# Kernel optimization log

Hardware: AMD Instinct MI355X
Metric: run time of the kernel (lower is better)

## Reference

```python
import jax, jax.numpy as jnp
import numpy as np

# Module hyperparameters (init_kwargs)
KH, KW = 1, 1            # kernel_size
PATCH_H, PATCH_W = 21, 21  # patch_size (displacement grid)
SH, SW = 1, 1            # stride
PAD_H, PAD_W = 0, 0      # padding
DILP_H, DILP_W = 1, 1    # dilation_patch
B, C, H, W = 8, 256, 64, 96


def setup_inputs() -> dict:
    key = jax.random.key(0)
    k1, k2 = jax.random.split(key)
    input1 = jax.random.normal(k1, (B, C, H, W), dtype=jnp.float32)
    input2 = jax.random.normal(k2, (B, C, H, W), dtype=jnp.float32)
    return {"input1": input1, "input2": input2}


def _correlation(x1, x2):
    """FlowNet-style spatial correlation (cost volume).

    out[b, pi, pj, i, j] = sum_{c, ki, kj}
        x1_pad[b, c, i*SH + ki, j*SW + kj] *
        x2_pad[b, c, i*SH + ki + (pi - radH)*DILP_H, j*SW + kj + (pj - radW)*DILP_W]
    Out-of-bounds reads of x2 are zero (handled by padding).
    """
    radH, radW = PATCH_H // 2, PATCH_W // 2
    x1p = jnp.pad(x1, ((0, 0), (0, 0), (PAD_H, PAD_H), (PAD_W, PAD_W)))
    x2p = jnp.pad(x2, ((0, 0), (0, 0),
                       (PAD_H + radH * DILP_H, PAD_H + radH * DILP_H),
                       (PAD_W + radW * DILP_W, PAD_W + radW * DILP_W)))
    Hp, Wp = H + 2 * PAD_H, W + 2 * PAD_W
    oH = (Hp - KH) // SH + 1
    oW = (Wp - KW) // SW + 1

    # displacement grid -> start offsets into x2p (0 corresponds to -rad shift)
    sh = jnp.arange(PATCH_H, dtype=jnp.int32) * DILP_H
    sw = jnp.arange(PATCH_W, dtype=jnp.int32) * DILP_W
    starts = jnp.stack(jnp.meshgrid(sh, sw, indexing="ij"), axis=-1).reshape(-1, 2)

    def step(carry, s):
        # shifted view of x2 aligned with padded x1
        sl = jax.lax.dynamic_slice(x2p, (0, 0, s[0], s[1]), (B, C, Hp, Wp))
        prod = jnp.sum(x1p * sl, axis=1)  # [B, Hp, Wp], channel reduction
        # kernel-window sum + output stride (KH=KW=1 -> single strided slice)
        acc = jnp.zeros((B, oH, oW), dtype=prod.dtype)
        for ki in range(KH):
            for kj in range(KW):
                acc = acc + jax.lax.slice(
                    prod, (0, ki, kj),
                    (B, ki + (oH - 1) * SH + 1, kj + (oW - 1) * SW + 1),
                    (1, SH, SW))
        return carry, acc

    _, out = jax.lax.scan(step, None, starts)  # [PATCH_H*PATCH_W, B, oH, oW]
    out = out.reshape(PATCH_H, PATCH_W, B, oH, oW)
    return jnp.transpose(out, (2, 0, 1, 3, 4))  # [B, patchH, patchW, oH, oW]


def reference(input1, input2):
    return _correlation(input1, input2)
```

## Files before the change

kernel.cpp:

```cpp
#include <hip/hip_runtime.h>

typedef __attribute__((ext_vector_type(8))) short short8;
typedef __attribute__((ext_vector_type(4))) float f32x4;
typedef __attribute__((ext_vector_type(4))) unsigned short us4;

constexpr int NB = 8, NC = 256, IH = 64, IW = 96;
constexpr int PATCH = 21, RAD = 10;
constexpr int TI = 8, TJ = 8;
constexpr int WIN = 28, NWIN = 784;
constexpr int KC = 32, NKS = NC / KC;
constexpr int PLANE = IH * IW;
constexpr int PH = IH + 2 * RAD, PW = IW + 2 * RAD;
constexpr int NBCH = NWIN * 4;
constexpr int NCHUNK = NBCH + 256;
constexpr int ASTR = IH * IW * KC;
constexpr int BSTR = PH * PW * KC;
constexpr size_t X1T_ELEMS = (size_t)NB * NKS * ASTR;
constexpr size_t X2P_ELEMS = (size_t)NB * NKS * BSTR;
constexpr int GSTR = 65;

__device__ __forceinline__ unsigned short f2bf(float f) {
  unsigned u = __builtin_bit_cast(unsigned, f);
  u += 0x7fffu + ((u >> 16) & 1u);
  return (unsigned short)(u >> 16);
}

__global__ __launch_bounds__(256) void x1_to_kmajor(
    const float* __restrict__ src, unsigned short* __restrict__ dst) {
  __shared__ float lsf[32 * 97];
  const int blk = blockIdx.x;
  const int ct = blk & 7, i = (blk >> 3) & 63, b = blk >> 9;
  const int c0 = ct * 32, t = threadIdx.x;
  const float* sp = src + ((size_t)b * NC + c0) * PLANE + (size_t)i * IW;
#pragma unroll
  for (int k = 0; k < 12; ++k) {
    int idx = k * 256 + t;
    int c = idx / 96, j = idx - c * 96;
    lsf[c * 97 + j] = sp[(size_t)c * PLANE + j];
  }
  __syncthreads();
  unsigned short* dp = dst + (((size_t)(b * NKS + ct) * IH + i) * IW) * KC;
#pragma unroll
  for (int k = 0; k < 3; ++k) {
    int o = k * 256 + t;
    int j = o >> 3, cq = o & 7;
    us4 v = {f2bf(lsf[(cq * 4 + 0) * 97 + j]), f2bf(lsf[(cq * 4 + 1) * 97 + j]),
             f2bf(lsf[(cq * 4 + 2) * 97 + j]), f2bf(lsf[(cq * 4 + 3) * 97 + j])};
    *(us4*)&dp[(size_t)j * KC + cq * 4] = v;
  }
}

__global__ __launch_bounds__(256) void x2_to_kmajor_pad(
    const float* __restrict__ src, unsigned short* __restrict__ dst) {
  __shared__ float lsf[32 * 97];
  const int blk = blockIdx.x;
  const int ct = blk & 7, i = (blk >> 3) % PH, b = blk / (PH * 8);
  const int c0 = ct * 32, t = threadIdx.x;
  const int isrc = i - RAD;
  const bool rowok = (unsigned)isrc < (unsigned)IH;
  if (rowok) {
    const float* sp = src + ((size_t)b * NC + c0) * PLANE + (size_t)isrc * IW;
#pragma unroll
    for (int k = 0; k < 12; ++k) {
      int idx = k * 256 + t;
      int c = idx / 96, j = idx - c * 96;
      lsf[c * 97 + j] = sp[(size_t)c * PLANE + j];
    }
  }
  __syncthreads();
  unsigned short* dp = dst + (((size_t)(b * NKS + ct) * PH + i) * PW) * KC;
#pragma unroll
  for (int k = 0; k < 4; ++k) {
    int o = k * 256 + t;
    if (o < PW * 8) {
      int j = o >> 3, cq = o & 7;
      int jsrc = j - RAD;
      us4 v = {0, 0, 0, 0};
      if (rowok && (unsigned)jsrc < (unsigned)IW)
        v = us4{f2bf(lsf[(cq * 4 + 0) * 97 + jsrc]), f2bf(lsf[(cq * 4 + 1) * 97 + jsrc]),
                f2bf(lsf[(cq * 4 + 2) * 97 + jsrc]), f2bf(lsf[(cq * 4 + 3) * 97 + jsrc])};
      *(us4*)&dp[(size_t)j * KC + cq * 4] = v;
    }
  }
}

__global__ __launch_bounds__(1024, 4) void corr_pipe16(
    const unsigned short* __restrict__ x1k, const unsigned short* __restrict__ x2k,
    float* __restrict__ out) {
  __shared__ __attribute__((aligned(16))) unsigned short ls[3 * NCHUNK * 8];

  const int t = threadIdx.x, lane = t & 63, wv = t >> 6;
  const int bid = blockIdx.x;
  const int b = bid & 7;
  const int tile = bid >> 3;
  const int ti = tile / 12, tj = tile - ti * 12;
  const int i0 = ti * TI, j0 = tj * TJ;
  const int mtp = wv & 1, cg = wv >> 1;
  const int cbeg = cg * 6;
  const int qk = lane >> 4, lr = lane & 15;

  const unsigned short* x1b = x1k + (size_t)b * NKS * ASTR;
  const unsigned short* x2b = x2k + (size_t)b * NKS * BSTR;

  const unsigned short* srcp[4];
#pragma unroll
  for (int it = 0; it < 4; ++it) {
    int q = it * 1024 + t;
    if (q < NBCH) {
      int w = ((q >> 3) << 1) | (((q >> 2) ^ (q >> 4)) & 1);
      int c4 = (q & 3) ^ (w & 3);
      int wi = w / WIN, wj = w - wi * WIN;
      srcp[it] = x2b + ((size_t)(i0 + wi) * PW + (j0 + wj)) * KC + c4 * 8;
    } else {
      int qa = (q - NBCH) & 255;
      int m = ((qa >> 3) << 1) | (((qa >> 2) ^ (qa >> 4)) & 1);
      int c4 = (qa & 3) ^ (m & 3);
      srcp[it] = x1b + ((size_t)(i0 + (m >> 3)) * IW + (j0 + (m & 7))) * KC + c4 * 8;
    }
  }

  f32x4 acc[2][7];
#pragma unroll
  for (int a = 0; a < 2; ++a)
#pragma unroll
    for (int cc = 0; cc < 7; ++cc) acc[a][cc] = (f32x4){0.f, 0.f, 0.f, 0.f};

#define STAGE(BUF, KS)                                                              \
  {                                                                                 \
    unsigned short* lb = &ls[(BUF) * NCHUNK * 8];                                   \
    _Pragma("unroll")                                                               \
    for (int it = 0; it < 3; ++it)                                                  \
      __builtin_amdgcn_global_load_lds(                                             \
          (const void*)(srcp[it] + (size_t)(KS) * BSTR),                            \
          (void*)(lb + (it * 1024 + wv * 64) * 8), 16, 0, 0);                       \
    if (wv < 5)                                                                     \
      __builtin_amdgcn_global_load_lds(                                             \
          (const void*)(srcp[3] + (size_t)(KS) * (wv == 0 ? BSTR : ASTR)),          \
          (void*)(lb + (3072 + wv * 64) * 8), 16, 0, 0);                            \
  }

#define COMPUTE(BUF)                                                                \
  {                                                                                 \
    const unsigned short* lb = &ls[(BUF) * NCHUNK * 8];                             \
    const int m0 = 32 * mtp + lr, m1 = m0 + 16;                                     \
    short8 a0 = *(const short8*)(lb + (NBCH + ((4 * m0 + qk) ^ (lr & 7))) * 8);     \
    short8 a1 = *(const short8*)(lb + (NBCH + ((4 * m1 + qk) ^ (lr & 7))) * 8);     \
    _Pragma("unroll")                                                               \
    for (int cc = 0; cc < 7; ++cc) {                                                \
      int wrow = 16 * (cbeg + cc) + lr;                                             \
      int slot = (4 * wrow + qk) ^ (lr & 7);                                        \
      short8 bf = *(const short8*)(lb + slot * 8);                                  \
      acc[0][cc] = __builtin_amdgcn_mfma_f32_16x16x32_bf16(a0, bf, acc[0][cc], 0, 0, 0); \
      acc[1][cc] = __builtin_amdgcn_mfma_f32_16x16x32_bf16(a1, bf, acc[1][cc], 0, 0, 0); \
    }                                                                               \
  }

  STAGE(0, 0)
  STAGE(1, 1)

#define ITER(KS, VMA, VMB)                                        \
  if ((KS) < 6) STAGE((KS + 2) % 3, KS + 2)                       \
  if (wv < 5) { asm volatile("s_waitcnt vmcnt(" #VMA ")" ::: "memory"); }  \
  else        { asm volatile("s_waitcnt vmcnt(" #VMB ")" ::: "memory"); }  \
  asm volatile("s_barrier" ::: "memory");                         \
  COMPUTE(KS % 3)                                                 \
  asm volatile("s_barrier" ::: "memory");

  ITER(0, 8, 6)
  ITER(1, 8, 6)
  ITER(2, 8, 6)
  ITER(3, 8, 6)
  ITER(4, 8, 6)
  ITER(5, 8, 6)
  ITER(6, 4, 3)
  ITER(7, 0, 0)
#undef ITER
#undef COMPUTE
#undef STAGE

  float* gf = (float*)ls;
#pragma unroll
  for (int ch = 0; ch < 2; ++ch) {
    __syncthreads();
    const int n0 = ch ? 384 : 0;
#pragma unroll
    for (int a = 0; a < 2; ++a)
#pragma unroll
      for (int cc = 0; cc < 7; ++cc) {
        int ccg = cbeg + cc;
        if (ch ? (ccg >= 24) : (ccg <= 24)) {
          int nl = 16 * ccg + lr - n0;
          int mb = 16 * (2 * mtp + a) + 4 * qk;
          float* gp = &gf[nl * GSTR + mb];
          gp[0] = acc[a][cc][0]; gp[1] = acc[a][cc][1];
          gp[2] = acc[a][cc][2]; gp[3] = acc[a][cc][3];
        }
      }
    __syncthreads();
    for (int s = t; s < 1764; s += 1024) {
      int pidx = s / 21, pj = s - pidx * 21;
      int ii = 0, rem = pidx, stop = 0;
#pragma unroll
      for (int k = 0; k < 7; ++k) {
        int cnt = ch ? (7 + k) : (14 - k);
        int go = (!stop) && (rem >= cnt);
        rem -= go ? cnt : 0;
        ii += go;
        stop |= !go;
      }
      int pi = ch ? (14 - ii + rem) : rem;
      int nl = 28 * (pi + ii) + pj - n0;
      int ms = 8 * ii;
      float g[8];
#pragma unroll
      for (int e = 0; e < 8; ++e) g[e] = gf[(nl + e) * GSTR + ms + e];
      float* op = out + ((((size_t)b * PATCH + pi) * PATCH + pj) * IH + (i0 + ii)) * IW + j0;
      f32x4 v0 = {g[0], g[1], g[2], g[3]};
      f32x4 v1 = {g[4], g[5], g[6], g[7]};
      *(f32x4*)op = v0;
      *(f32x4*)(op + 4) = v1;
    }
  }
}

constexpr int LDKF = 40;
__global__ __launch_bounds__(512, 2) void corr_mfma_fb(
    const float* __restrict__ x1, const float* __restrict__ x2, float* __restrict__ out) {
  __shared__ __attribute__((aligned(16))) unsigned short lsA[64 * LDKF];
  __shared__ __attribute__((aligned(16))) unsigned short lsB[NWIN * LDKF];
  const int t = threadIdx.x;
  const int b = blockIdx.y;
  const int ti = blockIdx.x / 12, tj = blockIdx.x % 12;
  const int i0 = ti * TI, j0 = tj * TJ;
  const int lane = t & 63, wv = t >> 6;
  const int mtp = wv >> 2, cg = wv & 3, cbeg = cg * 12;
  const int qk = lane >> 4, lr = lane & 15;
  f32x4 acc[2][13];
#pragma unroll
  for (int a = 0; a < 2; ++a)
#pragma unroll
    for (int cc = 0; cc < 13; ++cc) acc[a][cc] = (f32x4){0.f, 0.f, 0.f, 0.f};
  const int am = t & 63, ak4 = t >> 6;
  const int aii = am >> 3, ajj = am & 7;
  const float* x1p = x1 + ((size_t)b * NC + 4 * ak4) * PLANE + (size_t)(i0 + aii) * IW + (j0 + ajj);
  const float* x2b = x2 + (size_t)b * NC * PLANE;
  for (int ks = 0; ks < NKS; ++ks) {
    __syncthreads();
    {
      const float* p = x1p + (size_t)ks * KC * PLANE;
      us4 v = {f2bf(p[0]), f2bf(p[PLANE]), f2bf(p[2 * PLANE]), f2bf(p[3 * PLANE])};
      *(us4*)&lsA[am * LDKF + 4 * ak4] = v;
    }
    for (int w = t; w < NWIN; w += 512) {
      const int wi = w / WIN, wj = w - wi * WIN;
      const int gi = i0 - RAD + wi, gj = j0 - RAD + wj;
      const bool ok = ((unsigned)gi < (unsigned)IH) && ((unsigned)gj < (unsigned)IW);
      const float* p = x2b + ((size_t)(ks * KC) * IH + gi) * IW + gj;
      unsigned short* dst = &lsB[w * LDKF];
#pragma unroll
      for (int k4 = 0; k4 < 8; ++k4) {
        const float* q = p + (size_t)(4 * k4) * PLANE;
        us4 v = {f2bf(ok ? q[0] : 0.f), f2bf(ok ? q[PLANE] : 0.f),
                 f2bf(ok ? q[2 * PLANE] : 0.f), f2bf(ok ? q[3 * PLANE] : 0.f)};
        *(us4*)&dst[4 * k4] = v;
      }
    }
    __syncthreads();
    short8 a0 = *(const short8*)&lsA[(32 * mtp + lr) * LDKF + 8 * qk];
    short8 a1 = *(const short8*)&lsA[(32 * mtp + 16 + lr) * LDKF + 8 * qk];
#pragma unroll
    for (int cc = 0; cc < 13; ++cc) {
      const int wrow = 16 * (cbeg + cc) + lr;
      short8 bf = *(const short8*)&lsB[wrow * LDKF + 8 * qk];
      acc[0][cc] = __builtin_amdgcn_mfma_f32_16x16x32_bf16(a0, bf, acc[0][cc], 0, 0, 0);
      acc[1][cc] = __builtin_amdgcn_mfma_f32_16x16x32_bf16(a1, bf, acc[1][cc], 0, 0, 0);
    }
  }
#pragma unroll
  for (int a = 0; a < 2; ++a) {
    const int mb = 16 * (2 * mtp + a) + qk * 4;
#pragma unroll
    for (int cc = 0; cc < 13; ++cc) {
      if (cg > 0 && cc == 0) continue;
      const int n = 16 * (cbeg + cc) + lr;
      const int wi = n / WIN, wj = n - wi * WIN;
#pragma unroll
      for (int r = 0; r < 4; ++r) {
        const int m = mb + r;
        const int ii = m >> 3, jj = m & 7;
        const int pi = wi - ii, pj = wj - jj;
        if ((unsigned)pi < (unsigned)PATCH && (unsigned)pj < (unsigned)PATCH)
          out[((((size_t)b * PATCH + pi) * PATCH + pj) * IH + (i0 + ii)) * IW + (j0 + jj)] =
              acc[a][cc][r];
      }
    }
  }
}

extern "C" void kernel_launch(void* const* d_in, const int* in_sizes, int n_in,
                              void* d_out, int out_size, void* d_ws, size_t ws_size,
                              hipStream_t stream) {
  const float* x1 = (const float*)d_in[0];
  const float* x2 = (const float*)d_in[1];
  float* out = (float*)d_out;
  const size_t need = (X1T_ELEMS + X2P_ELEMS) * sizeof(unsigned short);
  if (ws_size >= need) {
    unsigned short* x1k = (unsigned short*)d_ws;
    unsigned short* x2k = x1k + X1T_ELEMS;
    x1_to_kmajor<<<NB * IH * 8, 256, 0, stream>>>(x1, x1k);
    x2_to_kmajor_pad<<<NB * PH * 8, 256, 0, stream>>>(x2, x2k);
    corr_pipe16<<<NB * 96, 1024, 0, stream>>>(x1k, x2k, out);
  } else {
    dim3 grid(96, NB);
    corr_mfma_fb<<<grid, 512, 0, stream>>>(x1, x2, out);
  }
}
```

Before: 95.13 us.

## Halve block to 8 waves, each wave covering all four M tiles

The correlation kernel now runs with 512 threads (8 waves) instead of 1024. Each wave keeps all four 16-row A fragments and 4x7 accumulators, so the B fragments loaded from LDS are reused across four MFMAs instead of two. Staging loads are redistributed with 7 source pointers per thread and a uniform vmcnt wait. This cuts LDS read traffic per MFMA but doubles accumulator registers and halves the number of waves available to hide latency.

New measurement: 86.13 us. -9.5%, faster.

```diff
diff --git a/kernel.cpp b/kernel.cpp
--- a/kernel.cpp
+++ b/kernel.cpp
@@ -84,7 +84,7 @@
   }
 }
 
-__global__ __launch_bounds__(1024, 4) void corr_pipe16(
+__global__ __launch_bounds__(512, 2) void corr_pipe8(
     const unsigned short* __restrict__ x1k, const unsigned short* __restrict__ x2k,
     float* __restrict__ out) {
   __shared__ __attribute__((aligned(16))) unsigned short ls[3 * NCHUNK * 8];
@@ -95,17 +95,16 @@
   const int tile = bid >> 3;
   const int ti = tile / 12, tj = tile - ti * 12;
   const int i0 = ti * TI, j0 = tj * TJ;
-  const int mtp = wv & 1, cg = wv >> 1;
-  const int cbeg = cg * 6;
+  const int cbeg = 6 * wv;
   const int qk = lane >> 4, lr = lane & 15;
 
   const unsigned short* x1b = x1k + (size_t)b * NKS * ASTR;
   const unsigned short* x2b = x2k + (size_t)b * NKS * BSTR;
 
-  const unsigned short* srcp[4];
-#pragma unroll
-  for (int it = 0; it < 4; ++it) {
-    int q = it * 1024 + t;
+  const unsigned short* srcp[7];
+#pragma unroll
+  for (int it = 0; it < 7; ++it) {
+    int q = it * 512 + t;
     if (q < NBCH) {
       int w = ((q >> 3) << 1) | (((q >> 2) ^ (q >> 4)) & 1);
       int c4 = (q & 3) ^ (w & 3);
@@ -119,9 +118,9 @@
     }
   }
 
-  f32x4 acc[2][7];
-#pragma unroll
-  for (int a = 0; a < 2; ++a)
+  f32x4 acc[4][7];
+#pragma unroll
+  for (int a = 0; a < 4; ++a)
 #pragma unroll
     for (int cc = 0; cc < 7; ++cc) acc[a][cc] = (f32x4){0.f, 0.f, 0.f, 0.f};
 
@@ -129,51 +128,53 @@
   {                                                                                 \
     unsigned short* lb = &ls[(BUF) * NCHUNK * 8];                                   \
     _Pragma("unroll")                                                               \
-    for (int it = 0; it < 3; ++it)                                                  \
+    for (int it = 0; it < 6; ++it)                                                  \
       __builtin_amdgcn_global_load_lds(                                             \
           (const void*)(srcp[it] + (size_t)(KS) * BSTR),                            \
-          (void*)(lb + (it * 1024 + wv * 64) * 8), 16, 0, 0);                       \
+          (void*)(lb + (it * 512 + wv * 64) * 8), 16, 0, 0);                        \
     if (wv < 5)                                                                     \
       __builtin_amdgcn_global_load_lds(                                             \
-          (const void*)(srcp[3] + (size_t)(KS) * (wv == 0 ? BSTR : ASTR)),          \
+          (const void*)(srcp[6] + (size_t)(KS) * (wv == 0 ? BSTR : ASTR)),          \
           (void*)(lb + (3072 + wv * 64) * 8), 16, 0, 0);                            \
   }
 
 #define COMPUTE(BUF)                                                                \
   {                                                                                 \
     const unsigned short* lb = &ls[(BUF) * NCHUNK * 8];                             \
-    const int m0 = 32 * mtp + lr, m1 = m0 + 16;                                     \
-    short8 a0 = *(const short8*)(lb + (NBCH + ((4 * m0 + qk) ^ (lr & 7))) * 8);     \
-    short8 a1 = *(const short8*)(lb + (NBCH + ((4 * m1 + qk) ^ (lr & 7))) * 8);     \
+    short8 af0 = *(const short8*)(lb + (NBCH + ((4 * (lr) + qk) ^ (lr & 7))) * 8);        \
+    short8 af1 = *(const short8*)(lb + (NBCH + ((4 * (16 + lr) + qk) ^ (lr & 7))) * 8);   \
+    short8 af2 = *(const short8*)(lb + (NBCH + ((4 * (32 + lr) + qk) ^ (lr & 7))) * 8);   \
+    short8 af3 = *(const short8*)(lb + (NBCH + ((4 * (48 + lr) + qk) ^ (lr & 7))) * 8);   \
     _Pragma("unroll")                                                               \
     for (int cc = 0; cc < 7; ++cc) {                                                \
       int wrow = 16 * (cbeg + cc) + lr;                                             \
       int slot = (4 * wrow + qk) ^ (lr & 7);                                        \
       short8 bf = *(const short8*)(lb + slot * 8);                                  \
-      acc[0][cc] = __builtin_amdgcn_mfma_f32_16x16x32_bf16(a0, bf, acc[0][cc], 0, 0, 0); \
-      acc[1][cc] = __builtin_amdgcn_mfma_f32_16x16x32_bf16(a1, bf, acc[1][cc], 0, 0, 0); \
+      acc[0][cc] = __builtin_amdgcn_mfma_f32_16x16x32_bf16(af0, bf, acc[0][cc], 0, 0, 0); \
+      acc[1][cc] = __builtin_amdgcn_mfma_f32_16x16x32_bf16(af1, bf, acc[1][cc], 0, 0, 0); \
+      acc[2][cc] = __builtin_amdgcn_mfma_f32_16x16x32_bf16(af2, bf, acc[2][cc], 0, 0, 0); \
+      acc[3][cc] = __builtin_amdgcn_mfma_f32_16x16x32_bf16(af3, bf, acc[3][cc], 0, 0, 0); \
     }                                                                               \
   }
 
   STAGE(0, 0)
   STAGE(1, 1)
 
-#define ITER(KS, VMA, VMB)                                        \
-  if ((KS) < 6) STAGE((KS + 2) % 3, KS + 2)                       \
-  if (wv < 5) { asm volatile("s_waitcnt vmcnt(" #VMA ")" ::: "memory"); }  \
-  else        { asm volatile("s_waitcnt vmcnt(" #VMB ")" ::: "memory"); }  \
-  asm volatile("s_barrier" ::: "memory");                         \
-  COMPUTE(KS % 3)                                                 \
+#define ITER(KS, VM)                                           \
+  if ((KS) < 6) STAGE((KS + 2) % 3, KS + 2)                    \
+  asm volatile("s_waitcnt vmcnt(" #VM ")" ::: "memory");       \
+  asm volatile("s_barrier" ::: "memory");                      \
+  COMPUTE(KS % 3)                                              \
   asm volatile("s_barrier" ::: "memory");
 
-  ITER(0, 8, 6)
-  ITER(1, 8, 6)
-  ITER(2, 8, 6)
-  ITER(3, 8, 6)
-  ITER(4, 8, 6)
-  ITER(5, 8, 6)
-  ITER(6, 4, 3)
-  ITER(7, 0, 0)
+  ITER(0, 12)
+  ITER(1, 12)
+  ITER(2, 12)
+  ITER(3, 12)
+  ITER(4, 12)
+  ITER(5, 12)
+  ITER(6, 6)
+  ITER(7, 0)
 #undef ITER
 #undef COMPUTE
 #undef STAGE
@@ -184,20 +185,20 @@
     __syncthreads();
     const int n0 = ch ? 384 : 0;
 #pragma unroll
-    for (int a = 0; a < 2; ++a)
+    for (int a = 0; a < 4; ++a)
 #pragma unroll
       for (int cc = 0; cc < 7; ++cc) {
         int ccg = cbeg + cc;
         if (ch ? (ccg >= 24) : (ccg <= 24)) {
           int nl = 16 * ccg + lr - n0;
-          int mb = 16 * (2 * mtp + a) + 4 * qk;
+          int mb = 16 * a + 4 * qk;
           float* gp = &gf[nl * GSTR + mb];
           gp[0] = acc[a][cc][0]; gp[1] = acc[a][cc][1];
           gp[2] = acc[a][cc][2]; gp[3] = acc[a][cc][3];
         }
       }
     __syncthreads();
-    for (int s = t; s < 1764; s += 1024) {
+    for (int s = t; s < 1764; s += 512) {
       int pidx = s / 21, pj = s - pidx * 21;
       int ii = 0, rem = pidx, stop = 0;
 #pragma unroll
@@ -309,7 +310,7 @@
     unsigned short* x2k = x1k + X1T_ELEMS;
     x1_to_kmajor<<<NB * IH * 8, 256, 0, stream>>>(x1, x1k);
     x2_to_kmajor_pad<<<NB * PH * 8, 256, 0, stream>>>(x2, x2k);
-    corr_pipe16<<<NB * 96, 1024, 0, stream>>>(x1k, x2k, out);
+    corr_pipe8<<<NB * 96, 512, 0, stream>>>(x1k, x2k, out);
   } else {
     dim3 grid(96, NB);
     corr_mfma_fb<<<grid, 512, 0, stream>>>(x1, x2, out);
```
